# Kernel tuning notes

Hardware: AMD Instinct MI355X
Metric: run time of the kernel (lower is better)

The kernel has to match this reference:

```python
import jax, jax.numpy as jnp
import numpy as np

S = 14
C = 20
STEP = 1.0 / 14
LAMBDA_COORD = 5.0
LAMBDA_NOOBJ = 0.5
EPS = 1e-7


def setup_inputs() -> dict:
    key = jax.random.key(0)
    k1, k2 = jax.random.split(key)
    pred = jax.random.uniform(k1, (4096, S, S, 10 + C), dtype=jnp.float32)
    target = jax.random.uniform(k2, (4096, S, S, 10 + C), dtype=jnp.float32)
    return {"pred": pred, "target": target}


def _convert_cell_box(box, ix, jy):
    # box: [..., 2, 4] in (cell-rel cx, cell-rel cy, w, h); returns clamped (x1, y1, w, h)
    x = (box[..., 0] + ix) * STEP - box[..., 2] / 2
    y = (box[..., 1] + jy) * STEP - box[..., 3] / 2
    out = jnp.stack([x, y, box[..., 2], box[..., 3]], axis=-1)
    return jnp.clip(out, 0.0)


def _paired_iou(b1, b2):
    # b1, b2: [..., 4] as (x, y, w, h)
    x1, y1, w1, h1 = b1[..., 0], b1[..., 1], b1[..., 2], b1[..., 3]
    x2, y2, w2, h2 = b2[..., 0], b2[..., 1], b2[..., 2], b2[..., 3]
    inter_w = w1 + w2 - (jnp.maximum(x1 + w1, x2 + w2) - jnp.minimum(x1, x2))
    inter_h = h1 + h2 - (jnp.maximum(y1 + h1, y2 + h2) - jnp.minimum(y1, y2))
    inter = jnp.clip(inter_w, 0.0) * jnp.clip(inter_h, 0.0)
    union = w1 * h1 + w2 * h2 - inter + EPS
    return inter / union


def _xywh_to_xyxy(box):
    cx, cy, w, h = box[..., 0], box[..., 1], box[..., 2], box[..., 3]
    return jnp.stack([cx - w / 2, cy - h / 2, cx + w / 2, cy + h / 2], axis=-1)


def _bbox_iou_xyxy(b1, b2):
    x1 = jnp.maximum(b1[..., 0], b2[..., 0])
    y1 = jnp.maximum(b1[..., 1], b2[..., 1])
    x2 = jnp.minimum(b1[..., 2], b2[..., 2])
    y2 = jnp.minimum(b1[..., 3], b2[..., 3])
    inter = jnp.clip(x2 - x1, 0.0) * jnp.clip(y2 - y1, 0.0)
    a1 = jnp.clip(b1[..., 2] - b1[..., 0], 0.0) * jnp.clip(b1[..., 3] - b1[..., 1], 0.0)
    a2 = jnp.clip(b2[..., 2] - b2[..., 0], 0.0) * jnp.clip(b2[..., 3] - b2[..., 1], 0.0)
    return inter / (a1 + a2 - inter + EPS)


def _yolo_loss(pred, target):
    N = pred.shape[0]
    dt = pred.dtype
    pb = pred[..., :10].reshape(N, S, S, 2, 5)
    tb = target[..., :10].reshape(N, S, S, 2, 5)
    pcls = pred[..., 10:]
    tcls = target[..., 10:]

    obj_mask = tb[..., 4] > 0          # [N,S,S,2]
    sig_mask = obj_mask[..., 1]        # [N,S,S]

    # grid offsets: dim1 is y (j), dim2 is x (i)
    ix = jnp.arange(S, dtype=dt)[None, None, :, None]
    jy = jnp.arange(S, dtype=dt)[None, :, None, None]
    p_conv = _convert_cell_box(pb[..., :4], ix, jy)
    t_conv = _convert_cell_box(tb[..., :4], ix, jy)
    ious = _paired_iou(p_conv, t_conv)          # [N,S,S,2]
    max_i = jnp.argmax(ious, axis=-1)           # [N,S,S]

    # where sig_mask: zero out the non-argmax anchor of obj_mask
    keep = (~sig_mask[..., None]) | (jnp.arange(2)[None, None, None, :] == max_i[..., None])
    obj_mask = obj_mask & keep

    fm = obj_mask.astype(dt)
    dconf2 = (pb[..., 4] - tb[..., 4]) ** 2
    obj_loss = jnp.sum(fm * dconf2)
    noobj_loss = jnp.sum((1.0 - fm) * dconf2)

    # Alpha-DIoU (alpha=0.5) over obj cells
    pxy = _xywh_to_xyxy(pb[..., :4])
    txy = _xywh_to_xyxy(tb[..., :4])
    iou = jnp.maximum(_bbox_iou_xyxy(pxy, txy), EPS)
    pcx = (pxy[..., 0] + pxy[..., 2]) / 2
    pcy = (pxy[..., 1] + pxy[..., 3]) / 2
    tcx = (txy[..., 0] + txy[..., 2]) / 2
    tcy = (txy[..., 1] + txy[..., 3]) / 2
    center_dist = (pcx - tcx) ** 2 + (pcy - tcy) ** 2
    ex1 = jnp.minimum(pxy[..., 0], txy[..., 0])
    ey1 = jnp.minimum(pxy[..., 1], txy[..., 1])
    ex2 = jnp.maximum(pxy[..., 2], txy[..., 2])
    ey2 = jnp.maximum(pxy[..., 3], txy[..., 3])
    diag = (ex2 - ex1) ** 2 + (ey2 - ey1) ** 2 + EPS
    diou_per = (1.0 - jnp.sqrt(iou)) + center_dist / diag
    n_obj = jnp.sum(fm)
    bbox_loss = jnp.where(n_obj > 0, jnp.sum(fm * diou_per) / jnp.maximum(n_obj, 1.0), 0.0)

    # Focal-MSE class loss over sig cells
    sm = sig_mask.astype(dt)
    ce = (pcls - tcls) ** 2
    pt = jnp.clip(jnp.exp(-ce), EPS, 1.0)
    focal = (1.0 - pt) ** 2 * ce
    n_cls = jnp.sum(sm) * C
    class_loss = jnp.where(n_cls > 0, jnp.sum(sm[..., None] * focal) / jnp.maximum(n_cls, 1.0), 0.0)

    total = obj_loss + LAMBDA_NOOBJ * noobj_loss + LAMBDA_COORD * bbox_loss + class_loss
    return total / N


def reference(pred, target):
    return _yolo_loss(pred, target)
```

## Files before the change

### kernel.cpp

```cpp
#include <hip/hip_runtime.h>
#include <math.h>


#define SGRID 14
#define NCLS 20
#define TILES_PER_WAVE 2
#define F4_PER_TILE 480

constexpr float STEPF  = 1.0f / 14.0f;
constexpr float EPSF   = 1e-7f;
constexpr float L_COORD = 5.0f;
constexpr float L_NOOBJ = 0.5f;

__device__ __forceinline__ float waveSum(float v) {
#pragma unroll
    for (int o = 32; o > 0; o >>= 1) v += __shfl_down(v, o);
    return v;
}

__device__ __forceinline__ void gload_lds16(const float4* gsrc, float4* ldst) {
    __builtin_amdgcn_global_load_lds(
        (const __attribute__((address_space(1))) void*)gsrc,
        (__attribute__((address_space(3))) void*)ldst, 16, 0, 0);
}

__global__ __launch_bounds__(256) void yolo_main(const float* __restrict__ pred,
                                                 const float* __restrict__ targ,
                                                 float* __restrict__ ws) {
    __shared__ float4 stage[4][2 * F4_PER_TILE];
    __shared__ float red[4][6];

    const int t = threadIdx.x;
    const int w = t >> 6;
    const int l = t & 63;

    float s[6] = {0.f, 0.f, 0.f, 0.f, 0.f, 0.f};

    const int gwave = blockIdx.x * 4 + w;
    float4* const wbuf = stage[w];

    const float4* pred4 = reinterpret_cast<const float4*>(pred);
    const float4* targ4 = reinterpret_cast<const float4*>(targ);

#pragma unroll
    for (int it = 0; it < TILES_PER_WAVE; ++it) {
        const int tile = gwave * TILES_PER_WAVE + it;

        asm volatile("s_waitcnt lgkmcnt(0)" ::: "memory");
        __builtin_amdgcn_sched_barrier(0);

        {
            const float4* psrc = pred4 + (size_t)tile * F4_PER_TILE;
            const float4* tsrc = targ4 + (size_t)tile * F4_PER_TILE;
#pragma unroll
            for (int i = 0; i < 15; ++i) {
                int g = i * 64 + l;
                const float4* src = (g < F4_PER_TILE) ? (psrc + g) : (tsrc + (g - F4_PER_TILE));
                gload_lds16(src, wbuf + i * 64);
            }
        }
        asm volatile("s_waitcnt vmcnt(0)" ::: "memory");
        __builtin_amdgcn_sched_barrier(0);

        float pv[30], tv[30];
        {
            const float2* cp = reinterpret_cast<const float2*>(wbuf) + l * 15;
            const float2* ct = reinterpret_cast<const float2*>(wbuf + F4_PER_TILE) + l * 15;
#pragma unroll
            for (int j = 0; j < 15; ++j) {
                float2 a = cp[j]; pv[2 * j] = a.x; pv[2 * j + 1] = a.y;
                float2 b = ct[j]; tv[2 * j] = b.x; tv[2 * j + 1] = b.y;
            }
        }

        const float* p = pv;
        const float* tt = tv;
        int cell = tile * 64 + l;
        float ix = (float)(cell % SGRID);
        float jy = (float)((cell / SGRID) % SGRID);

        float iouP[2];
#pragma unroll
        for (int b = 0; b < 2; ++b) {
            const float* pb = p + 5 * b;
            const float* tb = tt + 5 * b;
            float px = fmaxf((pb[0] + ix) * STEPF - pb[2] * 0.5f, 0.f);
            float py = fmaxf((pb[1] + jy) * STEPF - pb[3] * 0.5f, 0.f);
            float pw = fmaxf(pb[2], 0.f), ph = fmaxf(pb[3], 0.f);
            float tx = fmaxf((tb[0] + ix) * STEPF - tb[2] * 0.5f, 0.f);
            float ty = fmaxf((tb[1] + jy) * STEPF - tb[3] * 0.5f, 0.f);
            float tw = fmaxf(tb[2], 0.f), th = fmaxf(tb[3], 0.f);
            float iw = pw + tw - (fmaxf(px + pw, tx + tw) - fminf(px, tx));
            float ih = ph + th - (fmaxf(py + ph, ty + th) - fminf(py, ty));
            float inter = fmaxf(iw, 0.f) * fmaxf(ih, 0.f);
            float uni = pw * ph + tw * th - inter + EPSF;
            iouP[b] = inter / uni;
        }
        int maxi = (iouP[1] > iouP[0]) ? 1 : 0;
        bool sig = tt[9] > 0.f;

#pragma unroll
        for (int b = 0; b < 2; ++b) {
            const float* pb = p + 5 * b;
            const float* tb = tt + 5 * b;
            bool om = tb[4] > 0.f;
            bool kp = (!sig) || (b == maxi);
            float f = (om && kp) ? 1.f : 0.f;

            float d = pb[4] - tb[4];
            float d2 = d * d;
            s[0] += f * d2;
            s[1] += (1.f - f) * d2;

            float px1 = pb[0] - pb[2] * 0.5f, py1 = pb[1] - pb[3] * 0.5f;
            float px2 = pb[0] + pb[2] * 0.5f, py2 = pb[1] + pb[3] * 0.5f;
            float tx1 = tb[0] - tb[2] * 0.5f, ty1 = tb[1] - tb[3] * 0.5f;
            float tx2 = tb[0] + tb[2] * 0.5f, ty2 = tb[1] + tb[3] * 0.5f;

            float xi1 = fmaxf(px1, tx1), yi1 = fmaxf(py1, ty1);
            float xi2 = fminf(px2, tx2), yi2 = fminf(py2, ty2);
            float inter = fmaxf(xi2 - xi1, 0.f) * fmaxf(yi2 - yi1, 0.f);
            float a1 = fmaxf(px2 - px1, 0.f) * fmaxf(py2 - py1, 0.f);
            float a2 = fmaxf(tx2 - tx1, 0.f) * fmaxf(ty2 - ty1, 0.f);
            float iou = fmaxf(inter / (a1 + a2 - inter + EPSF), EPSF);

            float pcx = (px1 + px2) * 0.5f, pcy = (py1 + py2) * 0.5f;
            float tcx = (tx1 + tx2) * 0.5f, tcy = (ty1 + ty2) * 0.5f;
            float cd = (pcx - tcx) * (pcx - tcx) + (pcy - tcy) * (pcy - tcy);
            float ex1 = fminf(px1, tx1), ey1 = fminf(py1, ty1);
            float ex2 = fmaxf(px2, tx2), ey2 = fmaxf(py2, ty2);
            float diag = (ex2 - ex1) * (ex2 - ex1) + (ey2 - ey1) * (ey2 - ey1) + EPSF;
            float diou = 1.f - sqrtf(iou) + cd / diag;

            s[2] += f * diou;
            s[3] += f;
        }

        float fs = 0.f;
#pragma unroll
        for (int k = 0; k < NCLS; ++k) {
            float ce = p[10 + k] - tt[10 + k];
            ce *= ce;
            float pt = __expf(-ce);
            pt = fminf(fmaxf(pt, EPSF), 1.0f);
            float om1 = 1.f - pt;
            fs += om1 * om1 * ce;
        }
        float smv = sig ? 1.f : 0.f;
        s[4] += smv * fs;
        s[5] += smv;
    }

#pragma unroll
    for (int q = 0; q < 6; ++q) s[q] = waveSum(s[q]);
    if (l == 0) {
#pragma unroll
        for (int q = 0; q < 6; ++q) red[w][q] = s[q];
    }
    __syncthreads();
    if (t == 0) {
        float v[6];
#pragma unroll
        for (int q = 0; q < 6; ++q) v[q] = red[0][q] + red[1][q] + red[2][q] + red[3][q];
        float4* o = reinterpret_cast<float4*>(ws + (size_t)blockIdx.x * 8);
        o[0] = make_float4(v[0], v[1], v[2], v[3]);
        o[1] = make_float4(v[4], v[5], 0.f, 0.f);
    }
}

__global__ __launch_bounds__(256) void yolo_reduce(const float* __restrict__ ws,
                                                   float* __restrict__ out,
                                                   int nBlocks, float invN) {
    float s[6] = {0.f, 0.f, 0.f, 0.f, 0.f, 0.f};
    for (int row = threadIdx.x; row < nBlocks; row += 256) {
        const float4* r4 = reinterpret_cast<const float4*>(ws + (size_t)row * 8);
        float4 a = r4[0], b = r4[1];
        s[0] += a.x; s[1] += a.y; s[2] += a.z; s[3] += a.w; s[4] += b.x; s[5] += b.y;
    }
#pragma unroll
    for (int q = 0; q < 6; ++q) s[q] = waveSum(s[q]);

    __shared__ float red[4][6];
    int lane = threadIdx.x & 63;
    int wv   = threadIdx.x >> 6;
    if (lane == 0) {
#pragma unroll
        for (int q = 0; q < 6; ++q) red[wv][q] = s[q];
    }
    __syncthreads();
    if (threadIdx.x == 0) {
        float obj   = red[0][0] + red[1][0] + red[2][0] + red[3][0];
        float noobj = red[0][1] + red[1][1] + red[2][1] + red[3][1];
        float bboxS = red[0][2] + red[1][2] + red[2][2] + red[3][2];
        float nObj  = red[0][3] + red[1][3] + red[2][3] + red[3][3];
        float clsS  = red[0][4] + red[1][4] + red[2][4] + red[3][4];
        float smS   = red[0][5] + red[1][5] + red[2][5] + red[3][5];

        float bbox_loss = (nObj > 0.f) ? (bboxS / fmaxf(nObj, 1.f)) : 0.f;
        float nCls = smS * (float)NCLS;
        float class_loss = (nCls > 0.f) ? (clsS / fmaxf(nCls, 1.f)) : 0.f;
        float total = obj + L_NOOBJ * noobj + L_COORD * bbox_loss + class_loss;
        out[0] = total * invN;
    }
}

extern "C" void kernel_launch(void* const* d_in, const int* in_sizes, int n_in,
                              void* d_out, int out_size, void* d_ws, size_t ws_size,
                              hipStream_t stream) {
    const float* pred = (const float*)d_in[0];
    const float* targ = (const float*)d_in[1];
    float* out = (float*)d_out;
    float* ws = (float*)d_ws;

    int N = in_sizes[0] / (SGRID * SGRID * 30);
    int totalCells = N * SGRID * SGRID;
    int tiles = totalCells / 64;
    int gwaves = tiles / TILES_PER_WAVE;
    int blocks = gwaves / 4;

    yolo_main<<<blocks, 256, 0, stream>>>(pred, targ, ws);
    yolo_reduce<<<1, 256, 0, stream>>>(ws, out, blocks, 1.0f / (float)N);
}
```

Baseline: 39.66 us.

## Double-buffer LDS tile loads in a persistent grid-stride loop

Replaces the fixed two-tiles-per-wave launch with a persistent grid of 512 blocks of two waves, each striding over tiles. Each wave prefetches the next tile into a second LDS buffer with direct global-to-LDS loads while computing on the current one, waiting with a partial vmcnt. This is meant to overlap memory latency with compute. It hardcodes the tile count and 1/N for the 4096-batch input, so other sizes would give wrong results, and the small grid (1024 waves) may not give enough occupancy to keep memory busy.

```diff
diff --git a/kernel.cpp b/kernel.cpp
--- a/kernel.cpp
+++ b/kernel.cpp
@@ -4,8 +4,8 @@
 
 #define SGRID 14
 #define NCLS 20
-#define TILES_PER_WAVE 2
 #define F4_PER_TILE 480
+#define NT_TILES 12544
 
 constexpr float STEPF  = 1.0f / 14.0f;
 constexpr float EPSF   = 1e-7f;
@@ -24,11 +24,23 @@
         (__attribute__((address_space(3))) void*)ldst, 16, 0, 0);
 }
 
-__global__ __launch_bounds__(256) void yolo_main(const float* __restrict__ pred,
+__device__ __forceinline__ void issueTile(const float4* pred4, const float4* targ4,
+                                          int tile, int l, float4* dst) {
+    const float4* psrc = pred4 + (size_t)tile * F4_PER_TILE;
+    const float4* tsrc = targ4 + (size_t)tile * F4_PER_TILE;
+#pragma unroll
+    for (int i = 0; i < 15; ++i) {
+        int g = i * 64 + l;
+        const float4* src = (g < F4_PER_TILE) ? (psrc + g) : (tsrc + (g - F4_PER_TILE));
+        gload_lds16(src, dst + i * 64);
+    }
+}
+
+__global__ __launch_bounds__(128) void yolo_main(const float* __restrict__ pred,
                                                  const float* __restrict__ targ,
                                                  float* __restrict__ ws) {
-    __shared__ float4 stage[4][2 * F4_PER_TILE];
-    __shared__ float red[4][6];
+    __shared__ float4 stage[2][2][2 * F4_PER_TILE];
+    __shared__ float red[2][6];
 
     const int t = threadIdx.x;
     const int w = t >> 6;
@@ -36,31 +48,30 @@
 
     float s[6] = {0.f, 0.f, 0.f, 0.f, 0.f, 0.f};
 
-    const int gwave = blockIdx.x * 4 + w;
-    float4* const wbuf = stage[w];
+    const int G = gridDim.x * 2;
+    const int gwave = blockIdx.x * 2 + w;
 
     const float4* pred4 = reinterpret_cast<const float4*>(pred);
     const float4* targ4 = reinterpret_cast<const float4*>(targ);
 
-#pragma unroll
-    for (int it = 0; it < TILES_PER_WAVE; ++it) {
-        const int tile = gwave * TILES_PER_WAVE + it;
-
-        asm volatile("s_waitcnt lgkmcnt(0)" ::: "memory");
+    int buf = 0;
+    if (gwave < NT_TILES) issueTile(pred4, targ4, gwave, l, stage[w][0]);
+
+    for (int tile = gwave; tile < NT_TILES; tile += G) {
+        const int nxt = tile + G;
+
+        if (nxt < NT_TILES) {
+            asm volatile("s_waitcnt lgkmcnt(0)" ::: "memory");
+            __builtin_amdgcn_sched_barrier(0);
+            issueTile(pred4, targ4, nxt, l, stage[w][buf ^ 1]);
+            asm volatile("s_waitcnt vmcnt(15)" ::: "memory");
+        } else {
+            asm volatile("s_waitcnt vmcnt(0)" ::: "memory");
+        }
         __builtin_amdgcn_sched_barrier(0);
 
-        {
-            const float4* psrc = pred4 + (size_t)tile * F4_PER_TILE;
-            const float4* tsrc = targ4 + (size_t)tile * F4_PER_TILE;
-#pragma unroll
-            for (int i = 0; i < 15; ++i) {
-                int g = i * 64 + l;
-                const float4* src = (g < F4_PER_TILE) ? (psrc + g) : (tsrc + (g - F4_PER_TILE));
-                gload_lds16(src, wbuf + i * 64);
-            }
-        }
-        asm volatile("s_waitcnt vmcnt(0)" ::: "memory");
-        __builtin_amdgcn_sched_barrier(0);
+        const float4* wbuf = stage[w][buf];
+        buf ^= 1;
 
         float pv[30], tv[30];
         {
@@ -161,7 +172,7 @@
     if (t == 0) {
         float v[6];
 #pragma unroll
-        for (int q = 0; q < 6; ++q) v[q] = red[0][q] + red[1][q] + red[2][q] + red[3][q];
+        for (int q = 0; q < 6; ++q) v[q] = red[0][q] + red[1][q];
         float4* o = reinterpret_cast<float4*>(ws + (size_t)blockIdx.x * 8);
         o[0] = make_float4(v[0], v[1], v[2], v[3]);
         o[1] = make_float4(v[4], v[5], 0.f, 0.f);
@@ -213,11 +224,9 @@
     float* ws = (float*)d_ws;
 
     int N = in_sizes[0] / (SGRID * SGRID * 30);
-    int totalCells = N * SGRID * SGRID;
-    int tiles = totalCells / 64;
-    int gwaves = tiles / TILES_PER_WAVE;
-    int blocks = gwaves / 4;
-
-    yolo_main<<<blocks, 256, 0, stream>>>(pred, targ, ws);
-    yolo_reduce<<<1, 256, 0, stream>>>(ws, out, blocks, 1.0f / (float)N);
-}
+    (void)N;
+    int blocks = 512;
+
+    yolo_main<<<blocks, 128, 0, stream>>>(pred, targ, ws);
+    yolo_reduce<<<1, 256, 0, stream>>>(ws, out, blocks, 1.0f / 4096.0f);
+}
```

Result: no change. 39.12 us (-1.4%).
